# Kernel tuning notes

Measured on AMD Instinct MI355X. Metric: run time of the kernel, lower is better.

Reference implementation:

```python
import jax, jax.numpy as jnp
import numpy as np

EPS = 1e-12  # matches torch F.normalize default eps


def _idx(k, pad, stride, size):
    o = (size + 2 * pad - k) // stride + 1
    return (jnp.arange(o) * stride)[:, None] + jnp.arange(k)[None, :], o  # [o, k]


def unfold(x, k, pad, stride):
    # x: [B, C, H, W] -> [B, C*k*k, oh*ow], torch F.unfold ordering (c slowest, then kh, kw)
    B, C, H, W = x.shape
    xp = jnp.pad(x, ((0, 0), (0, 0), (pad, pad), (pad, pad)))
    ri, oh = _idx(k, pad, stride, H)
    ci, ow = _idx(k, pad, stride, W)
    p = xp[:, :, ri[:, None, :, None], ci[None, :, None, :]]  # [B, C, oh, ow, k, k]
    return p.transpose(0, 1, 4, 5, 2, 3).reshape(B, C * k * k, oh * ow)


def fold(cols, out_hw, k, pad, stride):
    # inverse of unfold with overlap-add (torch F.fold)
    B, CKK, L = cols.shape
    C = CKK // (k * k)
    H, W = out_hw
    ri, oh = _idx(k, pad, stride, H)
    ci, ow = _idx(k, pad, stride, W)
    p = cols.reshape(B, C, k, k, oh, ow).transpose(0, 1, 4, 5, 2, 3)  # [B,C,oh,ow,k,k]
    canvas = jnp.zeros((B, C, H + 2 * pad, W + 2 * pad), cols.dtype)
    canvas = canvas.at[:, :, ri[:, None, :, None], ci[None, :, None, :]].add(p)
    return canvas[:, :, pad:pad + H, pad:pad + W]


def _l2norm(x, axis):
    n = jnp.sqrt(jnp.sum(x * x, axis=axis, keepdims=True))
    return x / jnp.maximum(n, EPS)


def setup_inputs() -> dict:
    key = jax.random.key(0)
    ks = jax.random.split(key, 5)
    return {
        "lrsr_lv3": jax.random.normal(ks[0], (1, 256, 48, 48), jnp.float32),
        "refsr_lv3": jax.random.normal(ks[1], (1, 256, 48, 48), jnp.float32),
        "ref_lv1": jax.random.normal(ks[2], (1, 64, 192, 192), jnp.float32),
        "ref_lv2": jax.random.normal(ks[3], (1, 128, 96, 96), jnp.float32),
        "ref_lv3": jax.random.normal(ks[4], (1, 256, 48, 48), jnp.float32),
    }


def reference(lrsr_lv3, refsr_lv3, ref_lv1, ref_lv2, ref_lv3):
    B, C, H, W = lrsr_lv3.shape
    lr_u = unfold(lrsr_lv3, 3, 1, 1)              # [B, C*9, L_lr]
    rf_u = unfold(refsr_lv3, 3, 1, 1)             # [B, C*9, L_ref]
    rf_n = _l2norm(rf_u.transpose(0, 2, 1), 2)    # [B, L_ref, C*9]
    lr_n = _l2norm(lr_u, 1)                       # [B, C*9, L_lr]
    R = jnp.einsum('brc,bcl->brl', rf_n, lr_n)    # [B, L_ref, L_lr] cosine corr
    R_star = jnp.max(R, axis=1)                   # [B, L_lr]
    R_arg = jnp.argmax(R, axis=1)                 # [B, L_lr]

    ref3_u = unfold(ref_lv3, 3, 1, 1)             # [B, C*9,   L_ref]
    ref2_u = unfold(ref_lv2, 6, 2, 2)             # [B, C2*36, L_ref]
    ref1_u = unfold(ref_lv1, 12, 4, 4)            # [B, C1*144,L_ref]

    idx = R_arg[:, None, :]                       # [B, 1, L_lr]
    T3_u = jnp.take_along_axis(ref3_u, idx, axis=2)
    T2_u = jnp.take_along_axis(ref2_u, idx, axis=2)
    T1_u = jnp.take_along_axis(ref1_u, idx, axis=2)

    T_lv3 = fold(T3_u, (H, W), 3, 1, 1) / 9.0
    T_lv2 = fold(T2_u, (H * 2, W * 2), 6, 2, 2) / 9.0
    T_lv1 = fold(T1_u, (H * 4, W * 4), 12, 4, 4) / 9.0
    S = R_star.reshape(B, 1, H, W)
    return (S, T_lv3, T_lv2, T_lv1)
```

## Files before the change

kernel.cpp:

```cpp
#include <hip/hip_runtime.h>
#include <hip/hip_bf16.h>
#include <math.h>

#define HW 48
#define NPOS 2304
#define CCH 256
#define PCOLS 2500
#define PLANESZ (NPOS * CCH)
#define KC 16
#define TM 128
#define TN 64

typedef __attribute__((ext_vector_type(8))) short short8v;
typedef __attribute__((ext_vector_type(16))) float f32x16;

__device__ inline void ph_ss2(int vb, const float* __restrict__ lr,
                              const float* __restrict__ ref, float* __restrict__ SS2,
                              float (*red)[64]) {
    const int img = vb / 36, bx = vb % 36;
    const float* imgp = img ? ref : lr;
    const int t = threadIdx.x;
    const int px = t & 63, cg = t >> 6;
    const int p = bx * 64 + px;
    const float* base = imgp + (size_t)cg * 64 * NPOS + p;
    float s = 0.f;
#pragma unroll 4
    for (int cc = 0; cc < 64; ++cc) {
        float v = base[(size_t)cc * NPOS];
        s = fmaf(v, v, s);
    }
    red[cg][px] = s;
    __syncthreads();
    if (cg == 0)
        SS2[img * NPOS + p] = red[0][px] + red[1][px] + red[2][px] + red[3][px];
}

__device__ inline void ph_split(int local, const float* __restrict__ lr,
                                const float* __restrict__ ref, ushort* __restrict__ planes) {
    const int img = local / 288;
    const int gid = (local % 288) * 256 + threadIdx.x;
    const float* src = img ? ref : lr;
    const int lane = gid & 63;
    const int k16  = (gid >> 6) & 15;
    const int blk  = gid >> 10;
    const int pos  = blk * 32 + (lane & 31);
    const int c0   = k16 * 16 + (lane >> 5) * 8;
    ushort h8[8], m8[8], l8[8];
#pragma unroll
    for (int e = 0; e < 8; ++e) {
        float a = src[(size_t)(c0 + e) * NPOS + pos];
        __hip_bfloat16 hb = __float2bfloat16(a);
        float hf = __bfloat162float(hb);
        float r1 = a - hf;
        __hip_bfloat16 mb = __float2bfloat16(r1);
        float mf = __bfloat162float(mb);
        __hip_bfloat16 lb = __float2bfloat16(r1 - mf);
        h8[e] = *(ushort*)&hb;
        m8[e] = *(ushort*)&mb;
        l8[e] = *(ushort*)&lb;
    }
    ushort* ph = planes + (size_t)(img * 3 + 0) * PLANESZ + (size_t)gid * 8;
    ushort* pm = planes + (size_t)(img * 3 + 1) * PLANESZ + (size_t)gid * 8;
    ushort* pl = planes + (size_t)(img * 3 + 2) * PLANESZ + (size_t)gid * 8;
#pragma unroll
    for (int e = 0; e < 8; ++e) { ph[e] = h8[e]; pm[e] = m8[e]; pl[e] = l8[e]; }
}

__device__ inline void ph_zero(int local, float* __restrict__ P) {
    const int idx = local * 256 + threadIdx.x;
    if (idx >= NPOS * 196) return;
    const int row = idx / 196, b = idx - row * 196;
    int pc;
    if (b < 50)       pc = b;
    else if (b < 100) pc = 2450 + (b - 50);
    else {
        const int i = b - 100;
        const int rr = 1 + (i >> 1);
        pc = rr * 50 + ((i & 1) ? 49 : 0);
    }
    P[(size_t)row * PCOLS + pc] = 0.f;
}

__global__ __launch_bounds__(256) void prep_kernel(const float* __restrict__ lr,
                                                   const float* __restrict__ ref,
                                                   float* __restrict__ SS2,
                                                   ushort* __restrict__ planes,
                                                   float* __restrict__ P,
                                                   int do_split) {
    __shared__ float red[4][64];
    const int b = blockIdx.x;
    if (do_split) {
        if (b < 72)        ph_ss2(b, lr, ref, SS2, red);
        else if (b < 648)  ph_split(b - 72, lr, ref, planes);
        else               ph_zero(b - 648, P);
    } else {
        if (b < 72)        ph_ss2(b, lr, ref, SS2, red);
        else               ph_zero(b - 72, P);
    }
}

__device__ inline void ph_invnorm(int vb, const float* __restrict__ SS2,
                                  float* __restrict__ inv2) {
    const int img = vb / 9;
    const int p = (vb % 9) * 256 + threadIdx.x;
    const float* SS = SS2 + img * NPOS;
    const int y = p / HW, x = p % HW;
    float s = 0.f;
#pragma unroll
    for (int di = -1; di <= 1; ++di) {
        int yy = y + di;
        if ((unsigned)yy >= HW) continue;
#pragma unroll
        for (int dj = -1; dj <= 1; ++dj) {
            int xx = x + dj;
            if ((unsigned)xx >= HW) continue;
            s += SS[yy * HW + xx];
        }
    }
    inv2[img * NPOS + p] = 1.f / fmaxf(sqrtf(s), 1e-12f);
}

__device__ inline void ph_gemm(int g, const ushort* __restrict__ planes,
                               float* __restrict__ P) {
    const int bxg = g % 36, byg = g / 36;
    const int t = threadIdx.x, lane = t & 63, w = t >> 6;
    const int nblk0 = bxg * 2;
    const int ablk  = byg * 4 + w;

    const ushort* baseA  = planes + ((size_t)(ablk * 16) * 64 + lane) * 8;
    const ushort* baseB0 = planes + (size_t)3 * PLANESZ + ((size_t)(nblk0 * 16) * 64 + lane) * 8;
    const ushort* baseB1 = baseB0 + 16 * 64 * 8;

    f32x16 acc0 = {};
    f32x16 acc1 = {};
#pragma unroll 4
    for (int k = 0; k < 16; ++k) {
        const int fo = k * 512;
        short8v ah = *(const short8v*)(baseA + fo);
        short8v am = *(const short8v*)(baseA + PLANESZ + fo);
        short8v al = *(const short8v*)(baseA + 2 * PLANESZ + fo);
        short8v bh0 = *(const short8v*)(baseB0 + fo);
        short8v bm0 = *(const short8v*)(baseB0 + PLANESZ + fo);
        short8v bl0 = *(const short8v*)(baseB0 + 2 * PLANESZ + fo);
        short8v bh1 = *(const short8v*)(baseB1 + fo);
        short8v bm1 = *(const short8v*)(baseB1 + PLANESZ + fo);
        short8v bl1 = *(const short8v*)(baseB1 + 2 * PLANESZ + fo);
        acc0 = __builtin_amdgcn_mfma_f32_32x32x16_bf16(ah, bh0, acc0, 0, 0, 0);
        acc0 = __builtin_amdgcn_mfma_f32_32x32x16_bf16(ah, bm0, acc0, 0, 0, 0);
        acc0 = __builtin_amdgcn_mfma_f32_32x32x16_bf16(am, bh0, acc0, 0, 0, 0);
        acc0 = __builtin_amdgcn_mfma_f32_32x32x16_bf16(ah, bl0, acc0, 0, 0, 0);
        acc0 = __builtin_amdgcn_mfma_f32_32x32x16_bf16(al, bh0, acc0, 0, 0, 0);
        acc0 = __builtin_amdgcn_mfma_f32_32x32x16_bf16(am, bm0, acc0, 0, 0, 0);
        acc1 = __builtin_amdgcn_mfma_f32_32x32x16_bf16(ah, bh1, acc1, 0, 0, 0);
        acc1 = __builtin_amdgcn_mfma_f32_32x32x16_bf16(ah, bm1, acc1, 0, 0, 0);
        acc1 = __builtin_amdgcn_mfma_f32_32x32x16_bf16(am, bh1, acc1, 0, 0, 0);
        acc1 = __builtin_amdgcn_mfma_f32_32x32x16_bf16(ah, bl1, acc1, 0, 0, 0);
        acc1 = __builtin_amdgcn_mfma_f32_32x32x16_bf16(al, bh1, acc1, 0, 0, 0);
        acc1 = __builtin_amdgcn_mfma_f32_32x32x16_bf16(am, bm1, acc1, 0, 0, 0);
    }
    const int m0 = byg * 128 + w * 32;
    const int half = lane >> 5;
    const int colA = nblk0 * 32 + (lane & 31);
    const int colB = colA + 32;
    const int pcA = (colA / 48) * 50 + colA % 48 + 51;
    const int pcB = (colB / 48) * 50 + colB % 48 + 51;
#pragma unroll
    for (int r = 0; r < 16; ++r) {
        const int row = (r & 3) + 8 * (r >> 2) + 4 * half;
        P[(size_t)(m0 + row) * PCOLS + pcA] = acc0[r];
        P[(size_t)(m0 + row) * PCOLS + pcB] = acc1[r];
    }
}

__global__ __launch_bounds__(256) void corr_kernel(const float* __restrict__ SS2,
                                                   float* __restrict__ inv2,
                                                   const ushort* __restrict__ planes,
                                                   float* __restrict__ P,
                                                   int do_gemm) {
    const int b = blockIdx.x;
    if (b < 18)          ph_invnorm(b, SS2, inv2);
    else if (do_gemm)    ph_gemm(b - 18, planes, P);
}

__global__ __launch_bounds__(256) void gemm_p_kernel(const float* __restrict__ lr,
                                                     const float* __restrict__ ref,
                                                     float* __restrict__ P) {
    __shared__ float As[KC][TM];
    __shared__ float Bs[KC][TN];
    const int t  = threadIdx.x;
    const int tx = t & 15, ty = t >> 4;
    const int lp0 = blockIdx.y * TM, rp0 = blockIdx.x * TN;
    const int ac0 = t >> 5,        acol0 = (t & 31) << 2;
    const int ac1 = (t + 256) >> 5, acol1 = acol0;
    const int bc = t >> 4, bcol = (t & 15) << 2;
    float acc[8][4] = {};
    for (int c0 = 0; c0 < CCH; c0 += KC) {
        float4 a0 = *(const float4*)(lr  + (size_t)(c0 + ac0) * NPOS + lp0 + acol0);
        float4 a1 = *(const float4*)(lr  + (size_t)(c0 + ac1) * NPOS + lp0 + acol1);
        float4 b0 = *(const float4*)(ref + (size_t)(c0 + bc)  * NPOS + rp0 + bcol);
        __syncthreads();
        *(float4*)&As[ac0][acol0] = a0;
        *(float4*)&As[ac1][acol1] = a1;
        *(float4*)&Bs[bc][bcol]   = b0;
        __syncthreads();
#pragma unroll
        for (int kk = 0; kk < KC; ++kk) {
            float4 aA = *(const float4*)&As[kk][ty * 8];
            float4 aB = *(const float4*)&As[kk][ty * 8 + 4];
            float4 bb = *(const float4*)&Bs[kk][tx * 4];
            const float av[8] = {aA.x, aA.y, aA.z, aA.w, aB.x, aB.y, aB.z, aB.w};
            const float bv[4] = {bb.x, bb.y, bb.z, bb.w};
#pragma unroll
            for (int i = 0; i < 8; ++i)
#pragma unroll
                for (int j = 0; j < 4; ++j)
                    acc[i][j] = fmaf(av[i], bv[j], acc[i][j]);
        }
    }
    const int col0 = rp0 + tx * 4;
    const int pc0  = (col0 / 48) * 50 + (col0 % 48) + 51;
#pragma unroll
    for (int i = 0; i < 8; ++i) {
        const int m = lp0 + ty * 8 + i;
        float4 v = make_float4(acc[i][0], acc[i][1], acc[i][2], acc[i][3]);
        __builtin_memcpy(P + (size_t)m * PCOLS + pc0, &v, 16);
    }
}

__global__ __launch_bounds__(192) void maxarg_kernel(const float* __restrict__ P,
                                                     const float* __restrict__ inr,
                                                     const float* __restrict__ inl,
                                                     float* __restrict__ S,
                                                     int* __restrict__ arg) {
    const int l  = blockIdx.x;
    const int yl = l / HW, xl = l % HW;
    const int t  = threadIdx.x;

    bool vmask[9];
    const float* bp[9];
#pragma unroll
    for (int d = 0; d < 9; ++d) {
        const int di = d / 3 - 1, dj = d % 3 - 1;
        vmask[d] = ((unsigned)(yl + di) < HW) && ((unsigned)(xl + dj) < HW);
        bp[d] = P + (ptrdiff_t)(l + di * HW + dj) * PCOLS + (di * 50 + dj);
    }

    float best = -1e30f;
    int bestr = 0;
#pragma unroll
    for (int vv = 0; vv < 3; ++vv) {
        const int v   = t + vv * 192;
        const int yr  = v / 12;
        const int xr4 = (v - yr * 12) << 2;
        const int q0  = yr * 50 + xr4 + 51;
        const int r0  = yr * HW + xr4;
        float4 a = make_float4(0.f, 0.f, 0.f, 0.f);
#pragma unroll
        for (int d = 0; d < 9; ++d) {
            if (vmask[d]) {
                float4 x;
                __builtin_memcpy(&x, bp[d] + q0, 16);
                a.x += x.x; a.y += x.y; a.z += x.z; a.w += x.w;
            }
        }
        const float4 w = *(const float4*)(inr + r0);
        const float vals[4] = {a.x * w.x, a.y * w.y, a.z * w.z, a.w * w.w};
#pragma unroll
        for (int k = 0; k < 4; ++k)
            if (vals[k] > best) { best = vals[k]; bestr = r0 + k; }
    }

    __shared__ float bv[256];
    __shared__ int   br[256];
    bv[t] = best; br[t] = bestr;
    if (t < 64) { bv[192 + t] = -1e30f; br[192 + t] = 0; }
    __syncthreads();
    for (int s2 = 128; s2 > 0; s2 >>= 1) {
        if (t < s2) {
            float v2 = bv[t + s2]; int r2 = br[t + s2];
            if (v2 > bv[t] || (v2 == bv[t] && r2 < br[t])) { bv[t] = v2; br[t] = r2; }
        }
        __syncthreads();
    }
    if (t == 0) {
        S[l]   = bv[0] * inl[l];
        arg[l] = br[0];
    }
}

__global__ __launch_bounds__(256) void transposeT_kernel(const float* __restrict__ ref1,
                                                         const float* __restrict__ ref2,
                                                         const float* __restrict__ ref3,
                                                         float* __restrict__ T3t,
                                                         float* __restrict__ T2t,
                                                         float* __restrict__ T1t) {
    __shared__ float tile[64][65];
    const int b = blockIdx.x;
    const float* src; float* dst; int C, NPIX, tpx, tch;
    if (b < 144)      { src = ref3; dst = T3t; C = 256; NPIX = 2304;  tpx = b % 36;  tch = b / 36; }
    else if (b < 432) { const int lb = b - 144; src = ref2; dst = T2t; C = 128; NPIX = 9216;  tpx = lb % 144; tch = lb / 144; }
    else              { const int lb = b - 432; src = ref1; dst = T1t; C = 64;  NPIX = 36864; tpx = lb;       tch = 0; }
    const int t = threadIdx.x;
    const int px0 = tpx * 64, c0 = tch * 64;
#pragma unroll
    for (int r = 0; r < 16; ++r) {
        const int cl = r * 4 + (t >> 6), pl = t & 63;
        tile[cl][pl] = src[(size_t)(c0 + cl) * NPIX + px0 + pl];
    }
    __syncthreads();
#pragma unroll
    for (int r = 0; r < 16; ++r) {
        const int pl = r * 4 + (t >> 6), cl = t & 63;
        dst[(size_t)(px0 + pl) * C + c0 + cl] = tile[cl][pl];
    }
}

template <int S_, int C, int H>
__device__ inline void foldT(const float* __restrict__ refT, const int* __restrict__ arg,
                             float* __restrict__ out, int u, int lane) {
    const int y = u / 48, m = u % 48;
    const int ty_ = y / S_ + 1;
    float4 acc = make_float4(0.f, 0.f, 0.f, 0.f);
#pragma unroll
    for (int a = 0; a < 3; ++a) {
        const int oy = ty_ - a;
        if ((unsigned)oy >= HW) continue;
        const int di = y + S_ - S_ * oy;
#pragma unroll
        for (int b = 0; b < 3; ++b) {
            const int ox = m + 1 - b;
            if ((unsigned)ox >= HW) continue;
            const int ar = arg[oy * HW + ox];
            const int ry = ar / HW, rx = ar % HW;
            const int yy  = S_ * ry + di - S_;
            const int xx0 = S_ * (rx + b - 1);
            if ((unsigned)yy < H && (unsigned)xx0 < H) {
                float4 v;
                __builtin_memcpy(&v, refT + ((size_t)yy * H + xx0) * C + lane * 4, 16);
                acc.x += v.x; acc.y += v.y; acc.z += v.z; acc.w += v.w;
            }
        }
    }
    const int idx = lane * 4;
    const int xx = idx / C;
    const int c  = idx % C;
    const int x  = m * S_ + xx;
    const float vals[4] = {acc.x, acc.y, acc.z, acc.w};
    float* op = out + (size_t)c * (H * H) + (size_t)y * H + x;
#pragma unroll
    for (int e = 0; e < 4; ++e)
        op[(size_t)e * (H * H)] = vals[e] * (1.f / 9.f);
}

__global__ __launch_bounds__(256) void foldT_kernel(const float* __restrict__ T1t,
                                                    const float* __restrict__ T2t,
                                                    const float* __restrict__ T3t,
                                                    const int* __restrict__ argb,
                                                    float* __restrict__ T1,
                                                    float* __restrict__ T2,
                                                    float* __restrict__ T3) {
    const int b = blockIdx.x, w = threadIdx.x >> 6, lane = threadIdx.x & 63;
    if (b < 576)        foldT<1, 256, 48>(T3t, argb, T3, b * 4 + w, lane);
    else if (b < 1728)  foldT<2, 128, 96>(T2t, argb, T2, (b - 576) * 4 + w, lane);
    else                foldT<4, 64, 192>(T1t, argb, T1, (b - 1728) * 4 + w, lane);
}

extern "C" void kernel_launch(void* const* d_in, const int* in_sizes, int n_in,
                              void* d_out, int out_size, void* d_ws, size_t ws_size,
                              hipStream_t stream) {
    const float* lrsr  = (const float*)d_in[0];
    const float* refsr = (const float*)d_in[1];
    const float* ref1  = (const float*)d_in[2];
    const float* ref2  = (const float*)d_in[3];
    const float* ref3  = (const float*)d_in[4];

    float* out = (float*)d_out;
    float* S   = out;
    float* T3  = S  + NPOS;
    float* T2  = T3 + 256 * 48 * 48;
    float* T1  = T2 + 128 * 96 * 96;

    float*  P      = (float*)d_ws;
    float*  SS2    = P + (size_t)NPOS * PCOLS;
    float*  inv2   = SS2 + 2 * NPOS;
    int*    argb   = (int*)(inv2 + 2 * NPOS);
    ushort* planes = (ushort*)(argb + NPOS);
    float*  inl    = inv2;
    float*  inr    = inv2 + NPOS;

    float* T3t = P;
    float* T2t = T3t + 2304 * 256;
    float* T1t = T2t + 9216 * 128;

    const size_t need = ((size_t)NPOS * PCOLS + 5 * NPOS) * 4 + (size_t)6 * PLANESZ * 2;
    const int mfma_path = ws_size >= need ? 1 : 0;

    prep_kernel<<<mfma_path ? 2412 : 1836, 256, 0, stream>>>(lrsr, refsr, SS2, planes, P, mfma_path);

    if (mfma_path) {
        corr_kernel<<<666, 256, 0, stream>>>(SS2, inv2, planes, P, 1);
    } else {
        corr_kernel<<<18, 256, 0, stream>>>(SS2, inv2, planes, P, 0);
        gemm_p_kernel<<<dim3(NPOS / TN, NPOS / TM), 256, 0, stream>>>(lrsr, refsr, P);
    }

    maxarg_kernel<<<NPOS, 192, 0, stream>>>(P, inr, inl, S, argb);

    transposeT_kernel<<<1008, 256, 0, stream>>>(ref1, ref2, ref3, T3t, T2t, T1t);

    foldT_kernel<<<4032, 256, 0, stream>>>(T1t, T2t, T3t, argb, T1, T2, T3);
}
```

Measured before the change: 88.85 us.

## Merge NHWC transpose into prep kernel and stage fold outputs through LDS

When the workspace is large enough, the NHWC transposes of the reference features move into the prep kernel as extra blocks in a separate workspace region. This removes one kernel launch and lets the transposes overlap with the other prep work. The fold kernel now has each block process 16 output columns and stage the results in shared memory, so global stores become contiguous 16-byte writes instead of strided scalar stores. The cost is an extra sync and LDS traffic, and the transpose path depends on workspace size.

After: 90.65 us. +2.0%, slower.

```diff
diff --git a/kernel.cpp b/kernel.cpp
--- a/kernel.cpp
+++ b/kernel.cpp
@@ -81,22 +81,69 @@
     P[(size_t)row * PCOLS + pc] = 0.f;
 }
 
+__device__ inline void ph_transpose(int b, const float* __restrict__ ref1,
+                                    const float* __restrict__ ref2,
+                                    const float* __restrict__ ref3,
+                                    float* __restrict__ T3t, float* __restrict__ T2t,
+                                    float* __restrict__ T1t, float (*tile)[65]) {
+    const float* src; float* dst; int C, NPIX, tpx, tch;
+    if (b < 144)      { src = ref3; dst = T3t; C = 256; NPIX = 2304;  tpx = b % 36;  tch = b / 36; }
+    else if (b < 432) { const int lb = b - 144; src = ref2; dst = T2t; C = 128; NPIX = 9216;  tpx = lb % 144; tch = lb / 144; }
+    else              { const int lb = b - 432; src = ref1; dst = T1t; C = 64;  NPIX = 36864; tpx = lb;       tch = 0; }
+    const int t = threadIdx.x;
+    const int px0 = tpx * 64, c0 = tch * 64;
+#pragma unroll
+    for (int r = 0; r < 16; ++r) {
+        const int cl = r * 4 + (t >> 6), pl = t & 63;
+        tile[cl][pl] = src[(size_t)(c0 + cl) * NPIX + px0 + pl];
+    }
+    __syncthreads();
+#pragma unroll
+    for (int r = 0; r < 16; ++r) {
+        const int pl = r * 4 + (t >> 6), cl = t & 63;
+        dst[(size_t)(px0 + pl) * C + c0 + cl] = tile[cl][pl];
+    }
+}
+
 __global__ __launch_bounds__(256) void prep_kernel(const float* __restrict__ lr,
                                                    const float* __restrict__ ref,
+                                                   const float* __restrict__ ref1,
+                                                   const float* __restrict__ ref2,
+                                                   const float* __restrict__ ref3,
                                                    float* __restrict__ SS2,
                                                    ushort* __restrict__ planes,
                                                    float* __restrict__ P,
-                                                   int do_split) {
-    __shared__ float red[4][64];
+                                                   float* __restrict__ T3t,
+                                                   float* __restrict__ T2t,
+                                                   float* __restrict__ T1t,
+                                                   int do_split, int tbase) {
+    __shared__ union {
+        float red[4][64];
+        float tile[64][65];
+    } sm;
     const int b = blockIdx.x;
+    if (b >= tbase) {
+        ph_transpose(b - tbase, ref1, ref2, ref3, T3t, T2t, T1t, sm.tile);
+        return;
+    }
     if (do_split) {
-        if (b < 72)        ph_ss2(b, lr, ref, SS2, red);
+        if (b < 72)        ph_ss2(b, lr, ref, SS2, sm.red);
         else if (b < 648)  ph_split(b - 72, lr, ref, planes);
         else               ph_zero(b - 648, P);
     } else {
-        if (b < 72)        ph_ss2(b, lr, ref, SS2, red);
+        if (b < 72)        ph_ss2(b, lr, ref, SS2, sm.red);
         else               ph_zero(b - 72, P);
     }
+}
+
+__global__ __launch_bounds__(256) void transposeT_kernel(const float* __restrict__ ref1,
+                                                         const float* __restrict__ ref2,
+                                                         const float* __restrict__ ref3,
+                                                         float* __restrict__ T3t,
+                                                         float* __restrict__ T2t,
+                                                         float* __restrict__ T1t) {
+    __shared__ float tile[64][65];
+    ph_transpose(blockIdx.x, ref1, ref2, ref3, T3t, T2t, T1t, tile);
 }
 
 __device__ inline void ph_invnorm(int vb, const float* __restrict__ SS2,
@@ -288,81 +335,68 @@
     }
 }
 
-__global__ __launch_bounds__(256) void transposeT_kernel(const float* __restrict__ ref1,
-                                                         const float* __restrict__ ref2,
-                                                         const float* __restrict__ ref3,
-                                                         float* __restrict__ T3t,
-                                                         float* __restrict__ T2t,
-                                                         float* __restrict__ T1t) {
-    __shared__ float tile[64][65];
-    const int b = blockIdx.x;
-    const float* src; float* dst; int C, NPIX, tpx, tch;
-    if (b < 144)      { src = ref3; dst = T3t; C = 256; NPIX = 2304;  tpx = b % 36;  tch = b / 36; }
-    else if (b < 432) { const int lb = b - 144; src = ref2; dst = T2t; C = 128; NPIX = 9216;  tpx = lb % 144; tch = lb / 144; }
-    else              { const int lb = b - 432; src = ref1; dst = T1t; C = 64;  NPIX = 36864; tpx = lb;       tch = 0; }
-    const int t = threadIdx.x;
-    const int px0 = tpx * 64, c0 = tch * 64;
-#pragma unroll
-    for (int r = 0; r < 16; ++r) {
-        const int cl = r * 4 + (t >> 6), pl = t & 63;
-        tile[cl][pl] = src[(size_t)(c0 + cl) * NPIX + px0 + pl];
-    }
-    __syncthreads();
-#pragma unroll
-    for (int r = 0; r < 16; ++r) {
-        const int pl = r * 4 + (t >> 6), cl = t & 63;
-        dst[(size_t)(px0 + pl) * C + c0 + cl] = tile[cl][pl];
-    }
-}
-
 template <int S_, int C, int H>
-__device__ inline void foldT(const float* __restrict__ refT, const int* __restrict__ arg,
-                             float* __restrict__ out, int u, int lane) {
-    const int y = u / 48, m = u % 48;
+__device__ inline void fold2(const float* __restrict__ refT, const int* __restrict__ arg,
+                             float* __restrict__ out, int tileb, float* lds) {
+    const int y = tileb / 3, m0 = (tileb % 3) * 16;
+    const int t = threadIdx.x, w = t >> 6, lane = t & 63;
     const int ty_ = y / S_ + 1;
-    float4 acc = make_float4(0.f, 0.f, 0.f, 0.f);
-#pragma unroll
-    for (int a = 0; a < 3; ++a) {
-        const int oy = ty_ - a;
-        if ((unsigned)oy >= HW) continue;
-        const int di = y + S_ - S_ * oy;
-#pragma unroll
-        for (int b = 0; b < 3; ++b) {
-            const int ox = m + 1 - b;
-            if ((unsigned)ox >= HW) continue;
-            const int ar = arg[oy * HW + ox];
-            const int ry = ar / HW, rx = ar % HW;
-            const int yy  = S_ * ry + di - S_;
-            const int xx0 = S_ * (rx + b - 1);
-            if ((unsigned)yy < H && (unsigned)xx0 < H) {
-                float4 v;
-                __builtin_memcpy(&v, refT + ((size_t)yy * H + xx0) * C + lane * 4, 16);
-                acc.x += v.x; acc.y += v.y; acc.z += v.z; acc.w += v.w;
+#pragma unroll
+    for (int j = 0; j < 4; ++j) {
+        const int ul = w * 4 + j;
+        const int m = m0 + ul;
+        float4 acc = make_float4(0.f, 0.f, 0.f, 0.f);
+#pragma unroll
+        for (int a = 0; a < 3; ++a) {
+            const int oy = ty_ - a;
+            if ((unsigned)oy >= HW) continue;
+            const int di = y + S_ - S_ * oy;
+#pragma unroll
+            for (int b = 0; b < 3; ++b) {
+                const int ox = m + 1 - b;
+                if ((unsigned)ox >= HW) continue;
+                const int ar = arg[oy * HW + ox];
+                const int ry = ar / HW, rx = ar % HW;
+                const int yy  = S_ * ry + di - S_;
+                const int xx0 = S_ * (rx + b - 1);
+                if ((unsigned)yy < H && (unsigned)xx0 < H) {
+                    float4 v;
+                    __builtin_memcpy(&v, refT + ((size_t)yy * H + xx0) * C + lane * 4, 16);
+                    acc.x += v.x; acc.y += v.y; acc.z += v.z; acc.w += v.w;
+                }
             }
         }
-    }
-    const int idx = lane * 4;
-    const int xx = idx / C;
-    const int c  = idx % C;
-    const int x  = m * S_ + xx;
-    const float vals[4] = {acc.x, acc.y, acc.z, acc.w};
-    float* op = out + (size_t)c * (H * H) + (size_t)y * H + x;
-#pragma unroll
-    for (int e = 0; e < 4; ++e)
-        op[(size_t)e * (H * H)] = vals[e] * (1.f / 9.f);
-}
-
-__global__ __launch_bounds__(256) void foldT_kernel(const float* __restrict__ T1t,
+        const int idx = lane * 4;
+        const int xx = idx / C, c = idx % C;
+        float vals[4] = {acc.x * (1.f / 9.f), acc.y * (1.f / 9.f),
+                         acc.z * (1.f / 9.f), acc.w * (1.f / 9.f)};
+        __builtin_memcpy(&lds[(size_t)(ul * S_ + xx) * C + c], vals, 16);
+    }
+    __syncthreads();
+    const int c = t / S_, chunk = t % S_;
+    const int xb = m0 * S_ + chunk * 16;
+    float* op = out + (size_t)c * (H * H) + (size_t)y * H + xb;
+#pragma unroll
+    for (int q = 0; q < 4; ++q) {
+        float v4[4];
+#pragma unroll
+        for (int e = 0; e < 4; ++e) v4[e] = lds[(size_t)(chunk * 16 + q * 4 + e) * C + c];
+        __builtin_memcpy(op + q * 4, v4, 16);
+    }
+}
+
+__global__ __launch_bounds__(256) void fold2_kernel(const float* __restrict__ T1t,
                                                     const float* __restrict__ T2t,
                                                     const float* __restrict__ T3t,
                                                     const int* __restrict__ argb,
                                                     float* __restrict__ T1,
                                                     float* __restrict__ T2,
                                                     float* __restrict__ T3) {
-    const int b = blockIdx.x, w = threadIdx.x >> 6, lane = threadIdx.x & 63;
-    if (b < 576)        foldT<1, 256, 48>(T3t, argb, T3, b * 4 + w, lane);
-    else if (b < 1728)  foldT<2, 128, 96>(T2t, argb, T2, (b - 576) * 4 + w, lane);
-    else                foldT<4, 64, 192>(T1t, argb, T1, (b - 1728) * 4 + w, lane);
+    __shared__ float lds[4096];
+    const int b = blockIdx.x;
+    if (b < 144)      fold2<1, 256, 48>(T3t, argb, T3, b, lds);
+    else if (b < 432) fold2<2, 128, 96>(T2t, argb, T2, b - 144, lds);
+    else              fold2<4, 64, 192>(T1t, argb, T1, b - 432, lds);
 }
 
 extern "C" void kernel_launch(void* const* d_in, const int* in_sizes, int n_in,
@@ -388,14 +422,22 @@
     float*  inl    = inv2;
     float*  inr    = inv2 + NPOS;
 
-    float* T3t = P;
+    const size_t need  = ((size_t)NPOS * PCOLS + 5 * NPOS) * 4 + (size_t)6 * PLANESZ * 2;
+    const size_t nhwcB = (size_t)(2304 * 256 + 9216 * 128 + 36864 * 64) * 4;
+    const int mfma_path = ws_size >= need ? 1 : 0;
+    const int bigws     = ws_size >= need + nhwcB ? 1 : 0;
+
+    float* T3t = bigws ? (float*)((char*)d_ws + need) : P;
     float* T2t = T3t + 2304 * 256;
     float* T1t = T2t + 9216 * 128;
 
-    const size_t need = ((size_t)NPOS * PCOLS + 5 * NPOS) * 4 + (size_t)6 * PLANESZ * 2;
-    const int mfma_path = ws_size >= need ? 1 : 0;
-
-    prep_kernel<<<mfma_path ? 2412 : 1836, 256, 0, stream>>>(lrsr, refsr, SS2, planes, P, mfma_path);
+    {
+        const int tbase = mfma_path ? 2412 : 1836;
+        const int grid  = tbase + (bigws ? 1008 : 0);
+        prep_kernel<<<grid, 256, 0, stream>>>(lrsr, refsr, ref1, ref2, ref3,
+                                              SS2, planes, P, T3t, T2t, T1t,
+                                              mfma_path, bigws ? tbase : grid + 1);
+    }
 
     if (mfma_path) {
         corr_kernel<<<666, 256, 0, stream>>>(SS2, inv2, planes, P, 1);
@@ -406,7 +448,8 @@
 
     maxarg_kernel<<<NPOS, 192, 0, stream>>>(P, inr, inl, S, argb);
 
-    transposeT_kernel<<<1008, 256, 0, stream>>>(ref1, ref2, ref3, T3t, T2t, T1t);
-
-    foldT_kernel<<<4032, 256, 0, stream>>>(T1t, T2t, T3t, argb, T1, T2, T3);
-}
+    if (!bigws)
+        transposeT_kernel<<<1008, 256, 0, stream>>>(ref1, ref2, ref3, T3t, T2t, T1t);
+
+    fold2_kernel<<<1008, 256, 0, stream>>>(T1t, T2t, T3t, argb, T1, T2, T3);
+}
```
